# Kernel tuning notes

Measured on AMD Instinct MI355X. Metric: run time of the kernel, lower is better.

The kernel has to match this reference:

```python
import jax, jax.numpy as jnp
import numpy as np
import math

EPS = 1e-5
L2_EPS = 1e-12  # torch F.normalize default eps


def _bitlinear(x, W):
    """BitNet b1.58-style BitLinear: ternary weights (per-tensor mean-abs scale)
    and per-token int8 absmax activation quantization. No bias.
    x: [..., in], W: [out, in] -> [..., out]
    """
    w_scale = jnp.clip(jnp.mean(jnp.abs(W)), EPS, None)
    W_q = jnp.clip(jnp.round(W / w_scale), -1.0, 1.0) * w_scale
    x_scale = 127.0 / jnp.clip(jnp.max(jnp.abs(x), axis=-1, keepdims=True), EPS, None)
    x_q = jnp.clip(jnp.round(x * x_scale), -128.0, 127.0) / x_scale
    return jnp.einsum('bsi,oi->bso', x_q, W_q)


def setup_inputs() -> dict:
    key = jax.random.key(0)
    k1, k2, k3 = jax.random.split(key, 3)
    B, S, D_in, P, D_out = 4, 4096, 2048, 16, 2048
    x = jax.random.normal(k1, (B, S, D_in), dtype=jnp.float32)
    # xavier_normal_: std = sqrt(2 / (fan_in + fan_out))
    Wk = jax.random.normal(k2, (P, D_in), dtype=jnp.float32) * math.sqrt(2.0 / (D_in + P))
    Wv = jax.random.normal(k3, (D_out, P), dtype=jnp.float32) * math.sqrt(2.0 / (P + D_out))
    return {"x": x, "Wk": Wk, "Wv": Wv}


def reference(x, Wk, Wv):
    # key projection -> [B, S, P]
    attn = _bitlinear(x, Wk)
    # gelu (exact erf form, torch default) + L2-normalize * sqrt(P)
    attn = jax.nn.gelu(attn, approximate=False)
    norm = jnp.clip(jnp.linalg.norm(attn, axis=-1, keepdims=True), L2_EPS, None)
    attn = attn / norm * jnp.sqrt(jnp.float32(attn.shape[-1]))
    # value projection -> [B, S, D_out]
    return _bitlinear(attn, Wv)
```

## Files before the change

### kernel.cpp

```cpp
#include <hip/hip_runtime.h>

#define DIN   2048
#define DOUT  2048
#define NP    16
#define TPW   8
#define WPB   4

#define HDR_OFF   0
#define WK4_OFF   256
#define WV4_OFF   (WK4_OFF + 32768)

static __device__ __forceinline__ int dot4(unsigned a, unsigned b, int c) {
#if defined(__has_builtin) && __has_builtin(__builtin_amdgcn_sdot4)
  return __builtin_amdgcn_sdot4((int)a, (int)b, c, false);
#else
  c += (int)(signed char)(a & 0xffu)        * (int)(signed char)(b & 0xffu);
  c += (int)(signed char)((a >> 8) & 0xffu) * (int)(signed char)((b >> 8) & 0xffu);
  c += (int)(signed char)((a >> 16) & 0xffu)* (int)(signed char)((b >> 16) & 0xffu);
  c += (int)(signed char)(a >> 24)          * (int)(signed char)(b >> 24);
  return c;
#endif
}

static __device__ __forceinline__ unsigned qmagic(float f, float xs) {
  return __float_as_uint(fmaf(f, xs, 12582912.0f)) & 0xffu;
}

static __device__ __forceinline__ unsigned q8(float f, float xs) {
  float t = f * xs;
  float r = rintf(t);
  r = fmaxf(-128.0f, fminf(127.0f, r));
  return ((unsigned)(int)r) & 0xffu;
}

__global__ __launch_bounds__(256) void k_prep(
    const float* __restrict__ Wk, const float* __restrict__ Wv,
    float* __restrict__ hdr, unsigned* __restrict__ wk4, unsigned* __restrict__ wv4)
{
  __shared__ float red[8][256];
  const int tid = threadIdx.x, b = blockIdx.x;
  const int isV = (b >= 32);
  const float4* W = (const float4*)(isV ? Wv : Wk);

  float4 own = make_float4(0.f, 0.f, 0.f, 0.f);
#pragma unroll
  for (int lb = 0; lb < 8; ++lb) {
    float s = 0.f;
#pragma unroll
    for (int i = 0; i < 4; ++i) {
      float4 v = W[lb * 1024 + i * 256 + tid];
      if (!isV && (lb * 4 + i) == b) own = v;
      s += fabsf(v.x) + fabsf(v.y) + fabsf(v.z) + fabsf(v.w);
    }
    red[lb][tid] = s;
  }
  __syncthreads();
#pragma unroll 1
  for (int o = 128; o > 0; o >>= 1) {
    if (tid < o) {
#pragma unroll
      for (int lb = 0; lb < 8; ++lb) red[lb][tid] += red[lb][tid + o];
    }
    __syncthreads();
  }
  float sum = 0.f;
#pragma unroll
  for (int lb = 0; lb < 8; ++lb) sum += red[lb][0];
  const float sc = fmaxf(sum * (1.0f / 32768.0f), 1e-5f);
  if (tid == 0 && (b == 0 || b == 32)) hdr[isV] = sc;

  if (!isV) {
    const int c = b * 256 + tid;
    unsigned pk = 0; const float* wp = &own.x;
#pragma unroll
    for (int j = 0; j < 4; ++j) {
      float r = rintf(wp[j] / sc);
      r = fmaxf(-1.0f, fminf(1.0f, r));
      pk |= (((unsigned)(int)r) & 0xffu) << (8 * j);
    }
    wk4[c] = pk;
  } else {
    const int o = (b - 32) * 256 + tid;
    unsigned u[4];
#pragma unroll
    for (int cc = 0; cc < 4; ++cc) {
      float4 w = ((const float4*)Wv)[o * 4 + cc];
      const float* wp = &w.x;
      unsigned pk = 0;
#pragma unroll
      for (int r = 0; r < 4; ++r) {
        float q = rintf(wp[r] / sc);
        q = fmaxf(-1.0f, fminf(1.0f, q));
        pk |= (((unsigned)(int)q) & 0xffu) << (8 * r);
      }
      u[cc] = pk;
    }
    ((uint4*)wv4)[o] = make_uint4(u[0], u[1], u[2], u[3]);
  }
}

__global__ __launch_bounds__(256) void k_main(
    const float* __restrict__ x, const float* __restrict__ hdr,
    const unsigned* __restrict__ wk4, const unsigned* __restrict__ wv4,
    float* __restrict__ out)
{
  const int tid = threadIdx.x;
  const int l   = tid & 63;
  const int ws  = tid >> 6;
  const long t0 = ((long)blockIdx.x * WPB + ws) * TPW;

  __shared__ uint4 wkL[2048];
  __shared__ uint4 wvL[2048];
  __shared__ uint4 qls[WPB][TPW];
  __shared__ float sls[WPB][TPW];

  const float w1 = hdr[0], w2 = hdr[1];
  const float4* xf = (const float4*)x;

  float4 a[2][8];
#pragma unroll
  for (int c = 0; c < 8; ++c) a[0][c] = xf[t0 * 512 + c * 64 + l];

  {
    unsigned* wkW = (unsigned*)wkL;
#pragma unroll
    for (int i = 0; i < 32; ++i) {
      const int g = i * 256 + tid;
      const unsigned v = wk4[g];
      const int p = g >> 9, rem = g & 511, c = rem >> 6, lg = rem & 63;
      wkW[p * 512 + (c >> 2) * 256 + lg * 4 + (c & 3)] = v;
    }
#pragma unroll
    for (int i = 0; i < 8; ++i) {
      const int o = i * 256 + tid;
      const uint4 v = ((const uint4*)wv4)[o];
      const int m = o >> 8, r = o & 255, lr = r >> 2, j = r & 3;
      wvL[(m * 4 + j) * 64 + lr] = v;
    }
  }
  __syncthreads();

#pragma unroll 1
  for (int g = 0; g < TPW / 4; ++g) {
    int   sv[4];
    float s1[4];
#pragma unroll
    for (int ii = 0; ii < 4; ++ii) {
      const long tok = t0 + g * 4 + ii;

      float mx = 0.0f;
#pragma unroll
      for (int c = 0; c < 8; ++c) {
        float4 v = a[ii & 1][c];
        mx = fmaxf(mx, fabsf(v.x)); mx = fmaxf(mx, fabsf(v.y));
        mx = fmaxf(mx, fabsf(v.z)); mx = fmaxf(mx, fabsf(v.w));
      }
#pragma unroll
      for (int d = 1; d < 64; d <<= 1) mx = fmaxf(mx, __shfl_xor(mx, d, 64));
      const float mcl = fmaxf(mx, 1e-5f);
      const float xs  = 127.0f / mcl;
      s1[ii] = w1 / xs;

      unsigned qp[8];
#pragma unroll
      for (int c = 0; c < 8; ++c) {
        float4 v = a[ii & 1][c];
        qp[c] = qmagic(v.x, xs) | (qmagic(v.y, xs) << 8)
              | (qmagic(v.z, xs) << 16) | (qmagic(v.w, xs) << 24);
      }

      if (g * 4 + ii < TPW - 1) {
#pragma unroll
        for (int c = 0; c < 8; ++c)
          a[(ii + 1) & 1][c] = xf[(tok + 1) * 512 + c * 64 + l];
      }

      int acc[16];
#pragma unroll
      for (int p = 0; p < 16; ++p) {
        const uint4 w0 = wkL[p * 128 + l];
        const uint4 w4 = wkL[p * 128 + 64 + l];
        int d = 0;
        d = dot4(qp[0], w0.x, d); d = dot4(qp[1], w0.y, d);
        d = dot4(qp[2], w0.z, d); d = dot4(qp[3], w0.w, d);
        d = dot4(qp[4], w4.x, d); d = dot4(qp[5], w4.y, d);
        d = dot4(qp[6], w4.z, d); d = dot4(qp[7], w4.w, d);
        acc[p] = d;
      }

#pragma unroll
      for (int b = 0; b < 4; ++b) {
        const int lb = (l >> b) & 1;
#pragma unroll
        for (int j = 0; j < 8; ++j) {
          if (j < (8 >> b)) {
            int keep = lb ? acc[2 * j + 1] : acc[2 * j];
            int send = lb ? acc[2 * j]     : acc[2 * j + 1];
            acc[j] = keep + __shfl_xor(send, 1 << b, 64);
          }
        }
      }
      sv[ii] = acc[0];
    }

    const int lb4 = (l >> 4) & 1, lb5 = (l >> 5) & 1;
    int r0 = (lb4 ? sv[1] : sv[0]) + __shfl_xor(lb4 ? sv[0] : sv[1], 16, 64);
    int r1 = (lb4 ? sv[3] : sv[2]) + __shfl_xor(lb4 ? sv[2] : sv[3], 16, 64);
    int rr = (lb5 ? r1 : r0) + __shfl_xor(lb5 ? r0 : r1, 32, 64);
    float s1a = lb4 ? s1[1] : s1[0];
    float s1b = lb4 ? s1[3] : s1[2];
    const float s1sel = lb5 ? s1b : s1a;

    const float fa = (float)rr * s1sel;
    const float gv = 0.5f * fa * (1.0f + erff(fa * 0.70710678118654752f));
    float ss = gv * gv;
    ss += __shfl_xor(ss, 1, 64); ss += __shfl_xor(ss, 2, 64);
    ss += __shfl_xor(ss, 4, 64); ss += __shfl_xor(ss, 8, 64);
    const float rn = fmaxf(sqrtf(ss), 1e-12f);
    const float gn = gv * (4.0f / rn);
    float am = fabsf(gn);
    {
      float o;
      o = __shfl_xor(am, 1, 64); am = fmaxf(am, o);
      o = __shfl_xor(am, 2, 64); am = fmaxf(am, o);
      o = __shfl_xor(am, 4, 64); am = fmaxf(am, o);
      o = __shfl_xor(am, 8, 64); am = fmaxf(am, o);
    }
    const float mc2 = fmaxf(am, 1e-5f);
    const float xs2 = 127.0f / mc2;
    const float s2  = w2 / xs2;

    unsigned sh = q8(gn, xs2) << ((l & 3) * 8);
    sh |= (unsigned)__shfl_xor((int)sh, 1, 64);
    sh |= (unsigned)__shfl_xor((int)sh, 2, 64);
    const unsigned wa = (unsigned)__shfl_xor((int)sh, 4, 64);
    const unsigned wb = (unsigned)__shfl_xor((int)sh, 8, 64);
    const unsigned wc = (unsigned)__shfl_xor((int)sh, 12, 64);
    if ((l & 15) == 0) {
      qls[ws][g * 4 + (l >> 4)] = make_uint4(sh, wa, wb, wc);
      sls[ws][g * 4 + (l >> 4)] = s2;
    }
  }

  uint4 q[TPW]; float s2v[TPW];
#pragma unroll
  for (int i = 0; i < TPW; ++i) { q[i] = qls[ws][i]; s2v[i] = sls[ws][i]; }

#pragma unroll
  for (int m = 0; m < 8; ++m) {
    float h[TPW][4];
#pragma unroll
    for (int j = 0; j < 4; ++j) {
      const uint4 w = wvL[(m * 4 + j) * 64 + l];
#pragma unroll
      for (int t = 0; t < TPW; ++t) {
        int d = dot4(q[t].x, w.x, 0);
        d = dot4(q[t].y, w.y, d);
        d = dot4(q[t].z, w.z, d);
        d = dot4(q[t].w, w.w, d);
        h[t][j] = (float)d * s2v[t];
      }
    }
#pragma unroll
    for (int t = 0; t < TPW; ++t) {
      *(float4*)(out + (size_t)(t0 + t) * 2048 + m * 256 + l * 4) =
          make_float4(h[t][0], h[t][1], h[t][2], h[t][3]);
    }
  }
}

extern "C" void kernel_launch(void* const* d_in, const int* in_sizes, int n_in,
                              void* d_out, int out_size, void* d_ws, size_t ws_size,
                              hipStream_t stream) {
  const float* x  = (const float*)d_in[0];
  const float* Wk = (const float*)d_in[1];
  const float* Wv = (const float*)d_in[2];

  const int tokens = in_sizes[0] / DIN;

  char* ws = (char*)d_ws;
  float*    hdr = (float*)(ws + HDR_OFF);
  unsigned* wk4 = (unsigned*)(ws + WK4_OFF);
  unsigned* wv4 = (unsigned*)(ws + WV4_OFF);

  k_prep<<<40, 256, 0, stream>>>(Wk, Wv, hdr, wk4, wv4);
  k_main<<<tokens / (TPW * WPB), 256, 0, stream>>>(x, hdr, wk4, wv4, (float*)d_out);
}
```

Before: 249.4 us.

## Halve tokens per wave, read Wv from global, and raise occupancy

Halves tokens per wave (TPW 8→4) and drops the shared-memory copy of the ternary Wv. Wv is now pre-permuted in the prep kernel and read straight from global/L2 in the output loop. The Wk shared fill is rewritten as uint4 gathers, the x double-buffer prefetch is removed, and the per-token reduction is simplified. Launch bounds now request 4 blocks per CU. The aim is less LDS and fewer registers for higher occupancy, at the cost of less Wv reuse per load, losing the explicit x prefetch, and twice as many blocks each reloading Wk.

```diff
diff --git a/kernel.cpp b/kernel.cpp
--- a/kernel.cpp
+++ b/kernel.cpp
@@ -3,7 +3,7 @@
 #define DIN   2048
 #define DOUT  2048
 #define NP    16
-#define TPW   8
+#define TPW   4
 #define WPB   4
 
 #define HDR_OFF   0
@@ -95,13 +95,14 @@
       }
       u[cc] = pk;
     }
-    ((uint4*)wv4)[o] = make_uint4(u[0], u[1], u[2], u[3]);
-  }
-}
-
-__global__ __launch_bounds__(256) void k_main(
+    const int m = o >> 8, r = o & 255, lr = r >> 2, j = r & 3;
+    ((uint4*)wv4)[(m * 4 + j) * 64 + lr] = make_uint4(u[0], u[1], u[2], u[3]);
+  }
+}
+
+__global__ __launch_bounds__(256, 4) void k_main(
     const float* __restrict__ x, const float* __restrict__ hdr,
-    const unsigned* __restrict__ wk4, const unsigned* __restrict__ wv4,
+    const unsigned* __restrict__ wk4, const unsigned* __restrict__ wv4t,
     float* __restrict__ out)
 {
   const int tid = threadIdx.x;
@@ -110,108 +111,79 @@
   const long t0 = ((long)blockIdx.x * WPB + ws) * TPW;
 
   __shared__ uint4 wkL[2048];
-  __shared__ uint4 wvL[2048];
   __shared__ uint4 qls[WPB][TPW];
   __shared__ float sls[WPB][TPW];
 
   const float w1 = hdr[0], w2 = hdr[1];
-  const float4* xf = (const float4*)x;
-
-  float4 a[2][8];
-#pragma unroll
-  for (int c = 0; c < 8; ++c) a[0][c] = xf[t0 * 512 + c * 64 + l];
-
-  {
-    unsigned* wkW = (unsigned*)wkL;
-#pragma unroll
-    for (int i = 0; i < 32; ++i) {
-      const int g = i * 256 + tid;
-      const unsigned v = wk4[g];
-      const int p = g >> 9, rem = g & 511, c = rem >> 6, lg = rem & 63;
-      wkW[p * 512 + (c >> 2) * 256 + lg * 4 + (c & 3)] = v;
-    }
-#pragma unroll
-    for (int i = 0; i < 8; ++i) {
-      const int o = i * 256 + tid;
-      const uint4 v = ((const uint4*)wv4)[o];
-      const int m = o >> 8, r = o & 255, lr = r >> 2, j = r & 3;
-      wvL[(m * 4 + j) * 64 + lr] = v;
-    }
+  const float4* xf  = (const float4*)x;
+  const uint4*  wvt = (const uint4*)wv4t;
+
+#pragma unroll 1
+  for (int r = 0; r < 8; ++r) {
+    const int d = r * 256 + tid;
+    const int p = d >> 7, half = (d >> 6) & 1, lg = d & 63;
+    const int s = p * 512 + half * 256 + lg;
+    wkL[d] = make_uint4(wk4[s], wk4[s + 64], wk4[s + 128], wk4[s + 192]);
   }
   __syncthreads();
 
 #pragma unroll 1
-  for (int g = 0; g < TPW / 4; ++g) {
-    int   sv[4];
-    float s1[4];
-#pragma unroll
-    for (int ii = 0; ii < 4; ++ii) {
-      const long tok = t0 + g * 4 + ii;
-
-      float mx = 0.0f;
-#pragma unroll
-      for (int c = 0; c < 8; ++c) {
-        float4 v = a[ii & 1][c];
-        mx = fmaxf(mx, fabsf(v.x)); mx = fmaxf(mx, fabsf(v.y));
-        mx = fmaxf(mx, fabsf(v.z)); mx = fmaxf(mx, fabsf(v.w));
-      }
-#pragma unroll
-      for (int d = 1; d < 64; d <<= 1) mx = fmaxf(mx, __shfl_xor(mx, d, 64));
-      const float mcl = fmaxf(mx, 1e-5f);
-      const float xs  = 127.0f / mcl;
-      s1[ii] = w1 / xs;
-
-      unsigned qp[8];
-#pragma unroll
-      for (int c = 0; c < 8; ++c) {
-        float4 v = a[ii & 1][c];
-        qp[c] = qmagic(v.x, xs) | (qmagic(v.y, xs) << 8)
-              | (qmagic(v.z, xs) << 16) | (qmagic(v.w, xs) << 24);
-      }
-
-      if (g * 4 + ii < TPW - 1) {
-#pragma unroll
-        for (int c = 0; c < 8; ++c)
-          a[(ii + 1) & 1][c] = xf[(tok + 1) * 512 + c * 64 + l];
-      }
-
-      int acc[16];
-#pragma unroll
-      for (int p = 0; p < 16; ++p) {
-        const uint4 w0 = wkL[p * 128 + l];
-        const uint4 w4 = wkL[p * 128 + 64 + l];
-        int d = 0;
-        d = dot4(qp[0], w0.x, d); d = dot4(qp[1], w0.y, d);
-        d = dot4(qp[2], w0.z, d); d = dot4(qp[3], w0.w, d);
-        d = dot4(qp[4], w4.x, d); d = dot4(qp[5], w4.y, d);
-        d = dot4(qp[6], w4.z, d); d = dot4(qp[7], w4.w, d);
-        acc[p] = d;
-      }
-
-#pragma unroll
-      for (int b = 0; b < 4; ++b) {
-        const int lb = (l >> b) & 1;
-#pragma unroll
-        for (int j = 0; j < 8; ++j) {
-          if (j < (8 >> b)) {
-            int keep = lb ? acc[2 * j + 1] : acc[2 * j];
-            int send = lb ? acc[2 * j]     : acc[2 * j + 1];
-            acc[j] = keep + __shfl_xor(send, 1 << b, 64);
-          }
+  for (int t = 0; t < TPW; ++t) {
+    const long tok = t0 + t;
+
+    float4 a[8];
+#pragma unroll
+    for (int c = 0; c < 8; ++c) a[c] = xf[tok * 512 + c * 64 + l];
+
+    float mx = 0.0f;
+#pragma unroll
+    for (int c = 0; c < 8; ++c) {
+      mx = fmaxf(mx, fabsf(a[c].x)); mx = fmaxf(mx, fabsf(a[c].y));
+      mx = fmaxf(mx, fabsf(a[c].z)); mx = fmaxf(mx, fabsf(a[c].w));
+    }
+#pragma unroll
+    for (int d = 1; d < 64; d <<= 1) mx = fmaxf(mx, __shfl_xor(mx, d, 64));
+    const float mcl = fmaxf(mx, 1e-5f);
+    const float xs  = 127.0f / mcl;
+    const float s1  = w1 / xs;
+
+    unsigned qp[8];
+#pragma unroll
+    for (int c = 0; c < 8; ++c) {
+      qp[c] = qmagic(a[c].x, xs) | (qmagic(a[c].y, xs) << 8)
+            | (qmagic(a[c].z, xs) << 16) | (qmagic(a[c].w, xs) << 24);
+    }
+
+    int acc[16];
+#pragma unroll
+    for (int p = 0; p < 16; ++p) {
+      const uint4 w0 = wkL[p * 128 + l];
+      const uint4 w4 = wkL[p * 128 + 64 + l];
+      int d = 0;
+      d = dot4(qp[0], w0.x, d); d = dot4(qp[1], w0.y, d);
+      d = dot4(qp[2], w0.z, d); d = dot4(qp[3], w0.w, d);
+      d = dot4(qp[4], w4.x, d); d = dot4(qp[5], w4.y, d);
+      d = dot4(qp[6], w4.z, d); d = dot4(qp[7], w4.w, d);
+      acc[p] = d;
+    }
+
+#pragma unroll
+    for (int b = 0; b < 4; ++b) {
+      const int lb = (l >> b) & 1;
+#pragma unroll
+      for (int j = 0; j < 8; ++j) {
+        if (j < (8 >> b)) {
+          int keep = lb ? acc[2 * j + 1] : acc[2 * j];
+          int send = lb ? acc[2 * j]     : acc[2 * j + 1];
+          acc[j] = keep + __shfl_xor(send, 1 << b, 64);
         }
       }
-      sv[ii] = acc[0];
-    }
-
-    const int lb4 = (l >> 4) & 1, lb5 = (l >> 5) & 1;
-    int r0 = (lb4 ? sv[1] : sv[0]) + __shfl_xor(lb4 ? sv[0] : sv[1], 16, 64);
-    int r1 = (lb4 ? sv[3] : sv[2]) + __shfl_xor(lb4 ? sv[2] : sv[3], 16, 64);
-    int rr = (lb5 ? r1 : r0) + __shfl_xor(lb5 ? r0 : r1, 32, 64);
-    float s1a = lb4 ? s1[1] : s1[0];
-    float s1b = lb4 ? s1[3] : s1[2];
-    const float s1sel = lb5 ? s1b : s1a;
-
-    const float fa = (float)rr * s1sel;
+    }
+    int rr = acc[0];
+    rr += __shfl_xor(rr, 16, 64);
+    rr += __shfl_xor(rr, 32, 64);
+
+    const float fa = (float)rr * s1;
     const float gv = 0.5f * fa * (1.0f + erff(fa * 0.70710678118654752f));
     float ss = gv * gv;
     ss += __shfl_xor(ss, 1, 64); ss += __shfl_xor(ss, 2, 64);
@@ -236,9 +208,9 @@
     const unsigned wa = (unsigned)__shfl_xor((int)sh, 4, 64);
     const unsigned wb = (unsigned)__shfl_xor((int)sh, 8, 64);
     const unsigned wc = (unsigned)__shfl_xor((int)sh, 12, 64);
-    if ((l & 15) == 0) {
-      qls[ws][g * 4 + (l >> 4)] = make_uint4(sh, wa, wb, wc);
-      sls[ws][g * 4 + (l >> 4)] = s2;
+    if (l == 0) {
+      qls[ws][t] = make_uint4(sh, wa, wb, wc);
+      sls[ws][t] = s2;
     }
   }
 
@@ -246,25 +218,37 @@
 #pragma unroll
   for (int i = 0; i < TPW; ++i) { q[i] = qls[ws][i]; s2v[i] = sls[ws][i]; }
 
-#pragma unroll
+#pragma unroll 1
   for (int m = 0; m < 8; ++m) {
-    float h[TPW][4];
-#pragma unroll
-    for (int j = 0; j < 4; ++j) {
-      const uint4 w = wvL[(m * 4 + j) * 64 + l];
-#pragma unroll
-      for (int t = 0; t < TPW; ++t) {
-        int d = dot4(q[t].x, w.x, 0);
-        d = dot4(q[t].y, w.y, d);
-        d = dot4(q[t].z, w.z, d);
-        d = dot4(q[t].w, w.w, d);
-        h[t][j] = (float)d * s2v[t];
-      }
-    }
+    const uint4 wv0 = wvt[(m * 4 + 0) * 64 + l];
+    const uint4 wv1 = wvt[(m * 4 + 1) * 64 + l];
+    const uint4 wv2 = wvt[(m * 4 + 2) * 64 + l];
+    const uint4 wv3 = wvt[(m * 4 + 3) * 64 + l];
 #pragma unroll
     for (int t = 0; t < TPW; ++t) {
+      float h[4];
+      {
+        int d = dot4(q[t].x, wv0.x, 0);
+        d = dot4(q[t].y, wv0.y, d); d = dot4(q[t].z, wv0.z, d);
+        d = dot4(q[t].w, wv0.w, d); h[0] = (float)d * s2v[t];
+      }
+      {
+        int d = dot4(q[t].x, wv1.x, 0);
+        d = dot4(q[t].y, wv1.y, d); d = dot4(q[t].z, wv1.z, d);
+        d = dot4(q[t].w, wv1.w, d); h[1] = (float)d * s2v[t];
+      }
+      {
+        int d = dot4(q[t].x, wv2.x, 0);
+        d = dot4(q[t].y, wv2.y, d); d = dot4(q[t].z, wv2.z, d);
+        d = dot4(q[t].w, wv2.w, d); h[2] = (float)d * s2v[t];
+      }
+      {
+        int d = dot4(q[t].x, wv3.x, 0);
+        d = dot4(q[t].y, wv3.y, d); d = dot4(q[t].z, wv3.z, d);
+        d = dot4(q[t].w, wv3.w, d); h[3] = (float)d * s2v[t];
+      }
       *(float4*)(out + (size_t)(t0 + t) * 2048 + m * 256 + l * 4) =
-          make_float4(h[t][0], h[t][1], h[t][2], h[t][3]);
+          make_float4(h[0], h[1], h[2], h[3]);
     }
   }
 }
```

New measurement: 297.8 us. +19.4%, slower.
